# Performance work log

Measured on AMD Instinct MI355X. Metric: run time of the kernel, lower is better.

## Reference

```python
import jax, jax.numpy as jnp
from jax import lax
import numpy as np

SEQ_LEN, INPUT_DIM, HID, NCLS, BATCH = 1024, 1, 512, 10, 256


def setup_inputs() -> dict:
    key = jax.random.key(0)
    k1, k2, k3, k4 = jax.random.split(key, 4)
    def xavier(k, shape):
        fan_in, fan_out = shape[1], shape[0]
        bound = np.sqrt(6.0 / (fan_in + fan_out))
        return jax.random.uniform(k, shape, jnp.float32, -bound, bound)
    return {
        "x": jax.random.normal(k1, (BATCH, SEQ_LEN), jnp.float32),
        "h_init": jnp.zeros((HID, 1), jnp.float32),
        "W_hx": xavier(k2, (HID, INPUT_DIM)),
        "W_hh": xavier(k3, (HID, HID)),
        "b_h": jnp.zeros((HID, 1), jnp.float32),
        "W_ph": xavier(k4, (NCLS, HID)),
        "b_p": jnp.zeros((NCLS, 1), jnp.float32),
    }


def reference(x, h_init, W_hx, W_hh, b_h, W_ph, b_p):
    # x: [B, T] scalar inputs per step (input_dim == 1)
    B = x.shape[0]
    H = h_init.shape[0]
    # Broadcasting h_init [H,1] to [H,B] up-front is mathematically identical
    # to the torch code (W_hh @ h_init broadcasts against [H,B] at step 0).
    h0 = jnp.broadcast_to(h_init, (H, B))

    def step(h, x_t):
        # x_t: [B]; W_hx @ x_t[None,:] -> [H, B]
        h_new = jnp.tanh(W_hx @ x_t[None, :] + W_hh @ h + b_h)
        return h_new, None

    h_last, _ = lax.scan(step, h0, x.T)  # scan over time axis [T, B]
    p = W_ph @ h_last + b_p  # [NCLS, B]
    return p.T  # [B, NCLS]
```

## Files before the change

kernel.cpp:

```cpp
#include <hip/hip_runtime.h>


#define T_SEQ    1024
#define HID      512
#define NTHREADS 512
#define NW       8
#define NCLS     10
#define RP       8
#define PAIRS    32
#define PREG     28
#define PSTRIDE  576

typedef _Float16 half2_t __attribute__((ext_vector_type(2)));

__device__ __forceinline__ unsigned int pack2(float a, float b) {
    half2_t h = {(_Float16)a, (_Float16)b};
    return __builtin_bit_cast(unsigned int, h);
}

__device__ __forceinline__ float dot2(unsigned int w, unsigned int h, float acc) {
#if __has_builtin(__builtin_amdgcn_fdot2)
    return __builtin_amdgcn_fdot2(__builtin_bit_cast(half2_t, w),
                                  __builtin_bit_cast(half2_t, h), acc, false);
#else
    half2_t wv = __builtin_bit_cast(half2_t, w), hv = __builtin_bit_cast(half2_t, h);
    return acc + (float)wv.x * (float)hv.x + (float)wv.y * (float)hv.y;
#endif
}

__device__ __forceinline__ unsigned int bcast(unsigned int v, int lane) {
#if __has_builtin(__builtin_amdgcn_readlane)
    return __builtin_amdgcn_readlane(v, lane);
#else
    return __shfl((int)v, lane, 64);
#endif
}

__device__ __forceinline__ int pidx(int row) { return row + ((row >> 5) << 2); }

__device__ __forceinline__ float fast_tanh(float s) {
#if __has_builtin(__builtin_amdgcn_exp2f)
    float e = __builtin_amdgcn_exp2f(s * 2.885390081777927f);
#else
    float e = __expf(2.0f * s);
#endif
    return 1.0f - 2.0f / (e + 1.0f);
}

__global__ __attribute__((amdgpu_flat_work_group_size(NTHREADS, NTHREADS)))
           __attribute__((amdgpu_waves_per_eu(2, 2)))
void rnn_persist(
    const float* __restrict__ x, const float* __restrict__ h_init,
    const float* __restrict__ W_hx, const float* __restrict__ W_hh,
    const float* __restrict__ b_h, const float* __restrict__ W_ph,
    const float* __restrict__ b_p, float* __restrict__ out)
{
    __shared__ uint4    Wl4[NW * RP * 64];
    __shared__ float    part[2][NW][PSTRIDE];
    __shared__ float    x_s[T_SEQ];
    __shared__ _Float16 hs[HID];

    const int tid  = threadIdx.x;
    const int b    = blockIdx.x;
    const int w    = tid >> 6;
    const int lane = tid & 63;

    for (int i = tid; i < T_SEQ; i += NTHREADS) x_s[i] = x[(size_t)b * T_SEQ + i];

    const float whx = W_hx[tid];
    const float bh  = b_h[tid];
    const int   pi  = pidx(tid);
    hs[tid] = (_Float16)h_init[tid];

    unsigned int wreg[RP][PREG];
    #pragma unroll
    for (int r = 0; r < RP; ++r) {
        const float4* row = (const float4*)(W_hh + (size_t)(RP * lane + r) * HID + 64 * w);
        #pragma unroll
        for (int q = 0; q < 7; ++q) {
            float4 v = row[q];
            wreg[r][2 * q]     = pack2(v.x, v.y);
            wreg[r][2 * q + 1] = pack2(v.z, v.w);
        }
#if __has_builtin(__builtin_amdgcn_sched_barrier)
        __builtin_amdgcn_sched_barrier(0);
#endif
        #pragma unroll
        for (int q = 7; q < 14; ++q) {
            float4 v = row[q];
            wreg[r][2 * q]     = pack2(v.x, v.y);
            wreg[r][2 * q + 1] = pack2(v.z, v.w);
        }
        float4 v14 = row[14], v15 = row[15];
        Wl4[(w * RP + r) * 64 + lane] =
            make_uint4(pack2(v14.x, v14.y), pack2(v14.z, v14.w),
                       pack2(v15.x, v15.y), pack2(v15.z, v15.w));
#if __has_builtin(__builtin_amdgcn_sched_barrier)
        __builtin_amdgcn_sched_barrier(0);
#endif
    }

    #pragma unroll
    for (int r = 0; r < RP; ++r)
        #pragma unroll
        for (int p = 0; p < PREG; ++p)
            asm volatile("" : "+v"(wreg[r][p]));

    __syncthreads();

    const unsigned int* hs32 = (const unsigned int*)hs;
    float hval = 0.0f;

    #pragma unroll 1
    for (int t = 0; t < T_SEQ; ++t) {
        const int buf = t & 1;
        const float xw = x_s[t];

        unsigned int hpack = hs32[w * 32 + (lane & 31)];

        float acc[RP];
        #pragma unroll
        for (int r = 0; r < RP; ++r) acc[r] = 0.0f;

        #pragma unroll
        for (int p = 0; p < PREG; ++p) {
            unsigned int hp = bcast(hpack, p);
            #pragma unroll
            for (int r = 0; r < RP; ++r) acc[r] = dot2(wreg[r][p], hp, acc[r]);
        }
        {
            unsigned int hh0 = bcast(hpack, 28), hh1 = bcast(hpack, 29),
                         hh2 = bcast(hpack, 30), hh3 = bcast(hpack, 31);
            #pragma unroll
            for (int r = 0; r < RP; ++r) {
                uint4 wq = Wl4[(w * RP + r) * 64 + lane];
                acc[r] = dot2(wq.x, hh0, acc[r]);
                acc[r] = dot2(wq.y, hh1, acc[r]);
                acc[r] = dot2(wq.z, hh2, acc[r]);
                acc[r] = dot2(wq.w, hh3, acc[r]);
            }
        }

        *(float4*)&part[buf][w][pidx(RP * lane)]     = make_float4(acc[0], acc[1], acc[2], acc[3]);
        *(float4*)&part[buf][w][pidx(RP * lane + 4)] = make_float4(acc[4], acc[5], acc[6], acc[7]);

        __syncthreads();

        float s = whx * xw + bh;
        #pragma unroll
        for (int j = 0; j < NW; ++j) s += part[buf][j][pi];

        hval = fast_tanh(s);
        hs[tid] = (_Float16)hval;
    }

    __syncthreads();
    x_s[tid] = hval;
    __syncthreads();

    for (int c = w; c < NCLS; c += NW) {
        float s = 0.0f;
        #pragma unroll
        for (int j = 0; j < 8; ++j) {
            int r = lane + 64 * j;
            s += W_ph[c * HID + r] * x_s[r];
        }
        #pragma unroll
        for (int off = 32; off; off >>= 1) s += __shfl_down(s, off, 64);
        if (lane == 0) out[b * NCLS + c] = s + b_p[c];
    }
}

extern "C" void kernel_launch(void* const* d_in, const int* in_sizes, int n_in,
                              void* d_out, int out_size, void* d_ws, size_t ws_size,
                              hipStream_t stream) {
    const float* x      = (const float*)d_in[0];
    const float* h_init = (const float*)d_in[1];
    const float* W_hx   = (const float*)d_in[2];
    const float* W_hh   = (const float*)d_in[3];
    const float* b_h    = (const float*)d_in[4];
    const float* W_ph   = (const float*)d_in[5];
    const float* b_p    = (const float*)d_in[6];
    float* out = (float*)d_out;

    const int B = in_sizes[0] / T_SEQ;
    rnn_persist<<<B, NTHREADS, 0, stream>>>(x, h_init, W_hx, W_hh, b_h, W_ph, b_p, out);
}
```

Measured before the change: 1.435 ms.

## Split hidden rows between dot2 waves and MFMA waves with double-buffered state

Warps 0-3 keep the dot2 register-resident path for the first 256 hidden rows, and warps 4-7 compute the other 256 rows with 16x16x32 f16 MFMA using register-held A fragments, part of which spills to LDS. The hidden state is double-buffered in LDS and each step synchronizes with two raw s_barriers. The aim is to cut the per-step serial dot-product latency by moving half the matvec onto matrix cores and shrinking the partial-sum reduction. In exchange there are two barriers per step, MFMA waves where only one lane in 16 writes results, and a load imbalance between the two halves.

```diff
diff --git a/kernel.cpp b/kernel.cpp
--- a/kernel.cpp
+++ b/kernel.cpp
@@ -6,12 +6,25 @@
 #define NTHREADS 512
 #define NW       8
 #define NCLS     10
-#define RP       8
-#define PAIRS    32
-#define PREG     28
-#define PSTRIDE  576
+
+#define RV       256
+#define RPV      4
+#define PREG_V   56
+#define PSTRIDE  288
+
+#define NTILE    4
+#define KSTEPS   16
+#define KREG     14
 
 typedef _Float16 half2_t __attribute__((ext_vector_type(2)));
+typedef _Float16 half8_t __attribute__((ext_vector_type(8)));
+typedef float    f32x4_t __attribute__((ext_vector_type(4)));
+
+#if __has_builtin(__builtin_amdgcn_sched_barrier)
+#define SCHED_BARRIER() __builtin_amdgcn_sched_barrier(0)
+#else
+#define SCHED_BARRIER()
+#endif
 
 __device__ __forceinline__ unsigned int pack2(float a, float b) {
     half2_t h = {(_Float16)a, (_Float16)b};
@@ -47,6 +60,12 @@
     return 1.0f - 2.0f / (e + 1.0f);
 }
 
+__device__ __forceinline__ void wg_barrier() {
+    asm volatile("s_waitcnt lgkmcnt(0)" ::: "memory");
+    __builtin_amdgcn_s_barrier();
+    asm volatile("" ::: "memory");
+}
+
 __global__ __attribute__((amdgpu_flat_work_group_size(NTHREADS, NTHREADS)))
            __attribute__((amdgpu_waves_per_eu(2, 2)))
 void rnn_persist(
@@ -55,10 +74,12 @@
     const float* __restrict__ b_h, const float* __restrict__ W_ph,
     const float* __restrict__ b_p, float* __restrict__ out)
 {
-    __shared__ uint4    Wl4[NW * RP * 64];
-    __shared__ float    part[2][NW][PSTRIDE];
-    __shared__ float    x_s[T_SEQ];
-    __shared__ _Float16 hs[HID];
+    __shared__ __align__(16) float    x_s[T_SEQ];
+    __shared__ __align__(16) float    part[4][PSTRIDE];
+    __shared__ __align__(16) _Float16 hs[2][HID];
+    __shared__ uint4 WlA[4][RPV][64];
+    __shared__ uint4 WlB[4][RPV][64];
+    __shared__ uint4 Aspill[4][NTILE][2][64];
 
     const int tid  = threadIdx.x;
     const int b    = blockIdx.x;
@@ -66,96 +87,196 @@
     const int lane = tid & 63;
 
     for (int i = tid; i < T_SEQ; i += NTHREADS) x_s[i] = x[(size_t)b * T_SEQ + i];
-
-    const float whx = W_hx[tid];
-    const float bh  = b_h[tid];
-    const int   pi  = pidx(tid);
-    hs[tid] = (_Float16)h_init[tid];
-
-    unsigned int wreg[RP][PREG];
-    #pragma unroll
-    for (int r = 0; r < RP; ++r) {
-        const float4* row = (const float4*)(W_hh + (size_t)(RP * lane + r) * HID + 64 * w);
-        #pragma unroll
-        for (int q = 0; q < 7; ++q) {
-            float4 v = row[q];
-            wreg[r][2 * q]     = pack2(v.x, v.y);
-            wreg[r][2 * q + 1] = pack2(v.z, v.w);
-        }
-#if __has_builtin(__builtin_amdgcn_sched_barrier)
-        __builtin_amdgcn_sched_barrier(0);
-#endif
-        #pragma unroll
-        for (int q = 7; q < 14; ++q) {
-            float4 v = row[q];
-            wreg[r][2 * q]     = pack2(v.x, v.y);
-            wreg[r][2 * q + 1] = pack2(v.z, v.w);
-        }
-        float4 v14 = row[14], v15 = row[15];
-        Wl4[(w * RP + r) * 64 + lane] =
-            make_uint4(pack2(v14.x, v14.y), pack2(v14.z, v14.w),
-                       pack2(v15.x, v15.y), pack2(v15.z, v15.w));
-#if __has_builtin(__builtin_amdgcn_sched_barrier)
-        __builtin_amdgcn_sched_barrier(0);
-#endif
+    hs[0][tid] = (_Float16)h_init[tid];
+
+    if (w < 4) {
+        const float whx = W_hx[tid];
+        const float bh  = b_h[tid];
+        const int   pi  = pidx(tid);
+
+        unsigned int wreg[RPV][PREG_V];
+        #pragma unroll
+        for (int r = 0; r < RPV; ++r) {
+            const float* row = W_hh + (size_t)(RPV * lane + r) * HID + 128 * w;
+            #pragma unroll
+            for (int q = 0; q < 14; ++q) {
+                float4 v = *(const float4*)(row + 4 * q);
+                wreg[r][2 * q]     = pack2(v.x, v.y);
+                wreg[r][2 * q + 1] = pack2(v.z, v.w);
+            }
+            SCHED_BARRIER();
+            #pragma unroll
+            for (int q = 14; q < 28; ++q) {
+                float4 v = *(const float4*)(row + 4 * q);
+                wreg[r][2 * q]     = pack2(v.x, v.y);
+                wreg[r][2 * q + 1] = pack2(v.z, v.w);
+            }
+            float4 a0 = *(const float4*)(row + 112);
+            float4 a1 = *(const float4*)(row + 116);
+            WlA[w][r][lane] = make_uint4(pack2(a0.x, a0.y), pack2(a0.z, a0.w),
+                                         pack2(a1.x, a1.y), pack2(a1.z, a1.w));
+            float4 b0 = *(const float4*)(row + 120);
+            float4 b1 = *(const float4*)(row + 124);
+            WlB[w][r][lane] = make_uint4(pack2(b0.x, b0.y), pack2(b0.z, b0.w),
+                                         pack2(b1.x, b1.y), pack2(b1.z, b1.w));
+            SCHED_BARRIER();
+        }
+        #pragma unroll
+        for (int r = 0; r < RPV; ++r)
+            #pragma unroll
+            for (int p = 0; p < PREG_V; ++p)
+                asm volatile("" : "+v"(wreg[r][p]));
+
+        wg_barrier();
+
+        float hval = 0.0f;
+        #pragma unroll 1
+        for (int t = 0; t < T_SEQ; ++t) {
+            const int cur = t & 1;
+            const float xw = x_s[t];
+            unsigned int hpack = ((const unsigned int*)hs[cur])[64 * w + lane];
+
+            float acc[RPV] = {0.0f, 0.0f, 0.0f, 0.0f};
+            #pragma unroll
+            for (int p = 0; p < PREG_V; ++p) {
+                unsigned int hp = bcast(hpack, p);
+                #pragma unroll
+                for (int r = 0; r < RPV; ++r) acc[r] = dot2(wreg[r][p], hp, acc[r]);
+            }
+            {
+                unsigned int h0 = bcast(hpack, 56), h1 = bcast(hpack, 57),
+                             h2 = bcast(hpack, 58), h3 = bcast(hpack, 59);
+                #pragma unroll
+                for (int r = 0; r < RPV; ++r) {
+                    uint4 q = WlA[w][r][lane];
+                    acc[r] = dot2(q.x, h0, acc[r]);
+                    acc[r] = dot2(q.y, h1, acc[r]);
+                    acc[r] = dot2(q.z, h2, acc[r]);
+                    acc[r] = dot2(q.w, h3, acc[r]);
+                }
+                h0 = bcast(hpack, 60); h1 = bcast(hpack, 61);
+                h2 = bcast(hpack, 62); h3 = bcast(hpack, 63);
+                #pragma unroll
+                for (int r = 0; r < RPV; ++r) {
+                    uint4 q = WlB[w][r][lane];
+                    acc[r] = dot2(q.x, h0, acc[r]);
+                    acc[r] = dot2(q.y, h1, acc[r]);
+                    acc[r] = dot2(q.z, h2, acc[r]);
+                    acc[r] = dot2(q.w, h3, acc[r]);
+                }
+            }
+            *(float4*)&part[w][pidx(RPV * lane)] =
+                make_float4(acc[0], acc[1], acc[2], acc[3]);
+
+            wg_barrier();
+
+            float s = whx * xw + bh;
+            #pragma unroll
+            for (int j = 0; j < 4; ++j) s += part[j][pi];
+            hval = fast_tanh(s);
+            hs[cur ^ 1][tid] = (_Float16)hval;
+
+            wg_barrier();
+        }
+        x_s[tid] = hval;
+    } else {
+        const int widx  = w - 4;
+        const int g     = lane >> 4;
+        const int rloc  = lane & 15;
+        const int rbase = RV + 64 * widx;
+
+        half8_t afrag[NTILE][KREG];
+        float   whxr[NTILE][4], bhr[NTILE][4];
+        #pragma unroll
+        for (int tt = 0; tt < NTILE; ++tt) {
+            const float* rowp = W_hh + (size_t)(rbase + 16 * tt + rloc) * HID;
+            #pragma unroll
+            for (int ks = 0; ks < KREG; ++ks) {
+                float4 v0 = *(const float4*)(rowp + 32 * ks + 8 * g);
+                float4 v1 = *(const float4*)(rowp + 32 * ks + 8 * g + 4);
+                half8_t a = {(_Float16)v0.x, (_Float16)v0.y, (_Float16)v0.z, (_Float16)v0.w,
+                             (_Float16)v1.x, (_Float16)v1.y, (_Float16)v1.z, (_Float16)v1.w};
+                afrag[tt][ks] = a;
+                if (ks == 6) SCHED_BARRIER();
+            }
+            SCHED_BARRIER();
+            #pragma unroll
+            for (int ks = KREG; ks < KSTEPS; ++ks) {
+                float4 v0 = *(const float4*)(rowp + 32 * ks + 8 * g);
+                float4 v1 = *(const float4*)(rowp + 32 * ks + 8 * g + 4);
+                Aspill[widx][tt][ks - KREG][lane] =
+                    make_uint4(pack2(v0.x, v0.y), pack2(v0.z, v0.w),
+                               pack2(v1.x, v1.y), pack2(v1.z, v1.w));
+            }
+            #pragma unroll
+            for (int qq = 0; qq < 4; ++qq) {
+                const int rr = rbase + 16 * tt + 4 * g + qq;
+                whxr[tt][qq] = W_hx[rr];
+                bhr[tt][qq]  = b_h[rr];
+            }
+            SCHED_BARRIER();
+        }
+
+        f32x4_t acc[NTILE];
+        wg_barrier();
+
+        #pragma unroll 1
+        for (int t = 0; t < T_SEQ; ++t) {
+            const int cur = t & 1;
+            #pragma unroll
+            for (int tt = 0; tt < NTILE; ++tt) acc[tt] = (f32x4_t){0.f, 0.f, 0.f, 0.f};
+
+            #pragma unroll
+            for (int ks = 0; ks < KREG; ++ks) {
+                half8_t bf = *(const half8_t*)&hs[cur][32 * ks + 8 * g];
+                #pragma unroll
+                for (int tt = 0; tt < NTILE; ++tt)
+                    acc[tt] = __builtin_amdgcn_mfma_f32_16x16x32_f16(
+                                  afrag[tt][ks], bf, acc[tt], 0, 0, 0);
+            }
+            #pragma unroll
+            for (int ks = KREG; ks < KSTEPS; ++ks) {
+                half8_t bf = *(const half8_t*)&hs[cur][32 * ks + 8 * g];
+                #pragma unroll
+                for (int tt = 0; tt < NTILE; ++tt) {
+                    half8_t a = __builtin_bit_cast(half8_t,
+                                    Aspill[widx][tt][ks - KREG][lane]);
+                    acc[tt] = __builtin_amdgcn_mfma_f32_16x16x32_f16(
+                                  a, bf, acc[tt], 0, 0, 0);
+                }
+            }
+
+            const float xw = x_s[t];
+            if (rloc == 0) {
+                #pragma unroll
+                for (int tt = 0; tt < NTILE; ++tt) {
+                    float v0 = fast_tanh(acc[tt][0] + whxr[tt][0] * xw + bhr[tt][0]);
+                    float v1 = fast_tanh(acc[tt][1] + whxr[tt][1] * xw + bhr[tt][1]);
+                    float v2 = fast_tanh(acc[tt][2] + whxr[tt][2] * xw + bhr[tt][2]);
+                    float v3 = fast_tanh(acc[tt][3] + whxr[tt][3] * xw + bhr[tt][3]);
+                    *(uint2*)&hs[cur ^ 1][rbase + 16 * tt + 4 * g] =
+                        make_uint2(pack2(v0, v1), pack2(v2, v3));
+                }
+            }
+
+            wg_barrier();
+            wg_barrier();
+        }
+
+        const float xwl = x_s[T_SEQ - 1];
+        if (rloc == 0) {
+            #pragma unroll
+            for (int tt = 0; tt < NTILE; ++tt) {
+                float v0 = fast_tanh(acc[tt][0] + whxr[tt][0] * xwl + bhr[tt][0]);
+                float v1 = fast_tanh(acc[tt][1] + whxr[tt][1] * xwl + bhr[tt][1]);
+                float v2 = fast_tanh(acc[tt][2] + whxr[tt][2] * xwl + bhr[tt][2]);
+                float v3 = fast_tanh(acc[tt][3] + whxr[tt][3] * xwl + bhr[tt][3]);
+                *(float4*)&x_s[rbase + 16 * tt + 4 * g] =
+                    make_float4(v0, v1, v2, v3);
+            }
+        }
     }
 
-    #pragma unroll
-    for (int r = 0; r < RP; ++r)
-        #pragma unroll
-        for (int p = 0; p < PREG; ++p)
-            asm volatile("" : "+v"(wreg[r][p]));
-
-    __syncthreads();
-
-    const unsigned int* hs32 = (const unsigned int*)hs;
-    float hval = 0.0f;
-
-    #pragma unroll 1
-    for (int t = 0; t < T_SEQ; ++t) {
-        const int buf = t & 1;
-        const float xw = x_s[t];
-
-        unsigned int hpack = hs32[w * 32 + (lane & 31)];
-
-        float acc[RP];
-        #pragma unroll
-        for (int r = 0; r < RP; ++r) acc[r] = 0.0f;
-
-        #pragma unroll
-        for (int p = 0; p < PREG; ++p) {
-            unsigned int hp = bcast(hpack, p);
-            #pragma unroll
-            for (int r = 0; r < RP; ++r) acc[r] = dot2(wreg[r][p], hp, acc[r]);
-        }
-        {
-            unsigned int hh0 = bcast(hpack, 28), hh1 = bcast(hpack, 29),
-                         hh2 = bcast(hpack, 30), hh3 = bcast(hpack, 31);
-            #pragma unroll
-            for (int r = 0; r < RP; ++r) {
-                uint4 wq = Wl4[(w * RP + r) * 64 + lane];
-                acc[r] = dot2(wq.x, hh0, acc[r]);
-                acc[r] = dot2(wq.y, hh1, acc[r]);
-                acc[r] = dot2(wq.z, hh2, acc[r]);
-                acc[r] = dot2(wq.w, hh3, acc[r]);
-            }
-        }
-
-        *(float4*)&part[buf][w][pidx(RP * lane)]     = make_float4(acc[0], acc[1], acc[2], acc[3]);
-        *(float4*)&part[buf][w][pidx(RP * lane + 4)] = make_float4(acc[4], acc[5], acc[6], acc[7]);
-
-        __syncthreads();
-
-        float s = whx * xw + bh;
-        #pragma unroll
-        for (int j = 0; j < NW; ++j) s += part[buf][j][pi];
-
-        hval = fast_tanh(s);
-        hs[tid] = (_Float16)hval;
-    }
-
-    __syncthreads();
-    x_s[tid] = hval;
     __syncthreads();
 
     for (int c = w; c < NCLS; c += NW) {
```

New measurement: 2.474 ms. 72.4% more time.

## Batch 16 sequences per workgroup and compute recurrence with MFMA

Applied to the files above, without the earlier changes.

Replaces the per-sequence fdot2 recurrence with a 16-column batched MFMA formulation where each wave owns 64 full rows of W_hh in registers, removing the cross-wave partial-sum reduction and one barrier per step. Hidden states are double-buffered in LDS as fp16 and the input/bias term is folded into the accumulator init. Launches B/16 workgroups instead of B, so far fewer CUs are used and per-step latency depends on MFMA chain length.

```diff
diff --git a/kernel.cpp b/kernel.cpp
--- a/kernel.cpp
+++ b/kernel.cpp
@@ -6,37 +6,27 @@
 #define NTHREADS 512
 #define NW       8
 #define NCLS     10
-#define RP       8
-#define PAIRS    32
-#define PREG     28
-#define PSTRIDE  576
+#define COLS     16
+#define NTILE    4
+#define KSTEPS   16
+#define HSTR     520
+#define XSTR     1028
+#define HFSTR    516
 
 typedef _Float16 half2_t __attribute__((ext_vector_type(2)));
+typedef _Float16 half8_t __attribute__((ext_vector_type(8)));
+typedef float    f32x4_t __attribute__((ext_vector_type(4)));
+
+#if __has_builtin(__builtin_amdgcn_sched_barrier)
+#define SCHED_BARRIER() __builtin_amdgcn_sched_barrier(0)
+#else
+#define SCHED_BARRIER()
+#endif
 
 __device__ __forceinline__ unsigned int pack2(float a, float b) {
     half2_t h = {(_Float16)a, (_Float16)b};
     return __builtin_bit_cast(unsigned int, h);
 }
-
-__device__ __forceinline__ float dot2(unsigned int w, unsigned int h, float acc) {
-#if __has_builtin(__builtin_amdgcn_fdot2)
-    return __builtin_amdgcn_fdot2(__builtin_bit_cast(half2_t, w),
-                                  __builtin_bit_cast(half2_t, h), acc, false);
-#else
-    half2_t wv = __builtin_bit_cast(half2_t, w), hv = __builtin_bit_cast(half2_t, h);
-    return acc + (float)wv.x * (float)hv.x + (float)wv.y * (float)hv.y;
-#endif
-}
-
-__device__ __forceinline__ unsigned int bcast(unsigned int v, int lane) {
-#if __has_builtin(__builtin_amdgcn_readlane)
-    return __builtin_amdgcn_readlane(v, lane);
-#else
-    return __shfl((int)v, lane, 64);
-#endif
-}
-
-__device__ __forceinline__ int pidx(int row) { return row + ((row >> 5) << 2); }
 
 __device__ __forceinline__ float fast_tanh(float s) {
 #if __has_builtin(__builtin_amdgcn_exp2f)
@@ -49,125 +39,118 @@
 
 __global__ __attribute__((amdgpu_flat_work_group_size(NTHREADS, NTHREADS)))
            __attribute__((amdgpu_waves_per_eu(2, 2)))
-void rnn_persist(
+void rnn_mfma(
     const float* __restrict__ x, const float* __restrict__ h_init,
     const float* __restrict__ W_hx, const float* __restrict__ W_hh,
     const float* __restrict__ b_h, const float* __restrict__ W_ph,
     const float* __restrict__ b_p, float* __restrict__ out)
 {
-    __shared__ uint4    Wl4[NW * RP * 64];
-    __shared__ float    part[2][NW][PSTRIDE];
-    __shared__ float    x_s[T_SEQ];
-    __shared__ _Float16 hs[HID];
+    __shared__ __align__(16) _Float16 hs[2][COLS * HSTR];
+    __shared__ __align__(16) float    xs[COLS * XSTR];
+    __shared__ __align__(16) float    hfin[COLS * HFSTR];
 
     const int tid  = threadIdx.x;
-    const int b    = blockIdx.x;
     const int w    = tid >> 6;
     const int lane = tid & 63;
+    const int col  = lane & 15;
+    const int g    = lane >> 4;
+    const int col0 = blockIdx.x * COLS;
 
-    for (int i = tid; i < T_SEQ; i += NTHREADS) x_s[i] = x[(size_t)b * T_SEQ + i];
-
-    const float whx = W_hx[tid];
-    const float bh  = b_h[tid];
-    const int   pi  = pidx(tid);
-    hs[tid] = (_Float16)h_init[tid];
-
-    unsigned int wreg[RP][PREG];
-    #pragma unroll
-    for (int r = 0; r < RP; ++r) {
-        const float4* row = (const float4*)(W_hh + (size_t)(RP * lane + r) * HID + 64 * w);
-        #pragma unroll
-        for (int q = 0; q < 7; ++q) {
-            float4 v = row[q];
-            wreg[r][2 * q]     = pack2(v.x, v.y);
-            wreg[r][2 * q + 1] = pack2(v.z, v.w);
-        }
-#if __has_builtin(__builtin_amdgcn_sched_barrier)
-        __builtin_amdgcn_sched_barrier(0);
-#endif
-        #pragma unroll
-        for (int q = 7; q < 14; ++q) {
-            float4 v = row[q];
-            wreg[r][2 * q]     = pack2(v.x, v.y);
-            wreg[r][2 * q + 1] = pack2(v.z, v.w);
-        }
-        float4 v14 = row[14], v15 = row[15];
-        Wl4[(w * RP + r) * 64 + lane] =
-            make_uint4(pack2(v14.x, v14.y), pack2(v14.z, v14.w),
-                       pack2(v15.x, v15.y), pack2(v15.z, v15.w));
-#if __has_builtin(__builtin_amdgcn_sched_barrier)
-        __builtin_amdgcn_sched_barrier(0);
-#endif
+    for (int i = tid; i < COLS * T_SEQ; i += NTHREADS) {
+        const int c = i >> 10, t = i & (T_SEQ - 1);
+        xs[c * XSTR + t] = x[(size_t)(col0 + c) * T_SEQ + t];
+    }
+    for (int i = tid; i < COLS * HID; i += NTHREADS) {
+        const int c = i >> 9, r = i & (HID - 1);
+        hs[0][c * HSTR + r] = (_Float16)h_init[r];
     }
 
+    half8_t afrag[NTILE][KSTEPS];
+    float   whxr[NTILE][4], bhr[NTILE][4];
     #pragma unroll
-    for (int r = 0; r < RP; ++r)
+    for (int tt = 0; tt < NTILE; ++tt) {
+        const float* rowp = W_hh + (size_t)(64 * w + 16 * tt + col) * HID + 8 * g;
         #pragma unroll
-        for (int p = 0; p < PREG; ++p)
-            asm volatile("" : "+v"(wreg[r][p]));
+        for (int ks = 0; ks < KSTEPS; ++ks) {
+            float4 v0 = *(const float4*)(rowp + 32 * ks);
+            float4 v1 = *(const float4*)(rowp + 32 * ks + 4);
+            half8_t a = {(_Float16)v0.x, (_Float16)v0.y, (_Float16)v0.z, (_Float16)v0.w,
+                         (_Float16)v1.x, (_Float16)v1.y, (_Float16)v1.z, (_Float16)v1.w};
+            afrag[tt][ks] = a;
+            if ((ks & 3) == 3) SCHED_BARRIER();
+        }
+        #pragma unroll
+        for (int q = 0; q < 4; ++q) {
+            const int rr = 64 * w + 16 * tt + 4 * g + q;
+            whxr[tt][q] = W_hx[rr];
+            bhr[tt][q]  = b_h[rr];
+        }
+        SCHED_BARRIER();
+    }
+    #pragma unroll
+    for (int tt = 0; tt < NTILE; ++tt)
+        #pragma unroll
+        for (int ks = 0; ks < KSTEPS; ++ks)
+            asm volatile("" : "+v"(afrag[tt][ks]));
 
     __syncthreads();
 
-    const unsigned int* hs32 = (const unsigned int*)hs;
-    float hval = 0.0f;
-
     #pragma unroll 1
     for (int t = 0; t < T_SEQ; ++t) {
-        const int buf = t & 1;
-        const float xw = x_s[t];
+        const int cur = t & 1;
+        const _Float16* hb = &hs[cur][col * HSTR + 8 * g];
+        const float xw = xs[col * XSTR + t];
 
-        unsigned int hpack = hs32[w * 32 + (lane & 31)];
-
-        float acc[RP];
+        f32x4_t acc[NTILE];
         #pragma unroll
-        for (int r = 0; r < RP; ++r) acc[r] = 0.0f;
+        for (int tt = 0; tt < NTILE; ++tt) {
+            f32x4_t a0;
+            #pragma unroll
+            for (int q = 0; q < 4; ++q) a0[q] = whxr[tt][q] * xw + bhr[tt][q];
+            acc[tt] = a0;
+        }
 
         #pragma unroll
-        for (int p = 0; p < PREG; ++p) {
-            unsigned int hp = bcast(hpack, p);
+        for (int ks = 0; ks < KSTEPS; ++ks) {
+            half8_t bf = *(const half8_t*)(hb + 32 * ks);
             #pragma unroll
-            for (int r = 0; r < RP; ++r) acc[r] = dot2(wreg[r][p], hp, acc[r]);
-        }
-        {
-            unsigned int hh0 = bcast(hpack, 28), hh1 = bcast(hpack, 29),
-                         hh2 = bcast(hpack, 30), hh3 = bcast(hpack, 31);
-            #pragma unroll
-            for (int r = 0; r < RP; ++r) {
-                uint4 wq = Wl4[(w * RP + r) * 64 + lane];
-                acc[r] = dot2(wq.x, hh0, acc[r]);
-                acc[r] = dot2(wq.y, hh1, acc[r]);
-                acc[r] = dot2(wq.z, hh2, acc[r]);
-                acc[r] = dot2(wq.w, hh3, acc[r]);
-            }
+            for (int tt = 0; tt < NTILE; ++tt)
+                acc[tt] = __builtin_amdgcn_mfma_f32_16x16x32_f16(
+                              afrag[tt][ks], bf, acc[tt], 0, 0, 0);
         }
 
-        *(float4*)&part[buf][w][pidx(RP * lane)]     = make_float4(acc[0], acc[1], acc[2], acc[3]);
-        *(float4*)&part[buf][w][pidx(RP * lane + 4)] = make_float4(acc[4], acc[5], acc[6], acc[7]);
+        _Float16* hn = &hs[cur ^ 1][col * HSTR];
+        #pragma unroll
+        for (int tt = 0; tt < NTILE; ++tt) {
+            const float v0 = fast_tanh(acc[tt][0]);
+            const float v1 = fast_tanh(acc[tt][1]);
+            const float v2 = fast_tanh(acc[tt][2]);
+            const float v3 = fast_tanh(acc[tt][3]);
+            *(uint2*)&hn[64 * w + 16 * tt + 4 * g] =
+                make_uint2(pack2(v0, v1), pack2(v2, v3));
+            if (t == T_SEQ - 1)
+                *(float4*)&hfin[col * HFSTR + 64 * w + 16 * tt + 4 * g] =
+                    make_float4(v0, v1, v2, v3);
+        }
 
         __syncthreads();
-
-        float s = whx * xw + bh;
-        #pragma unroll
-        for (int j = 0; j < NW; ++j) s += part[buf][j][pi];
-
-        hval = fast_tanh(s);
-        hs[tid] = (_Float16)hval;
     }
 
-    __syncthreads();
-    x_s[tid] = hval;
-    __syncthreads();
-
-    for (int c = w; c < NCLS; c += NW) {
-        float s = 0.0f;
-        #pragma unroll
-        for (int j = 0; j < 8; ++j) {
-            int r = lane + 64 * j;
-            s += W_ph[c * HID + r] * x_s[r];
+    {
+        const int sub = lane >> 5, l32 = lane & 31;
+        const int cl  = 2 * w + sub;
+        #pragma unroll 1
+        for (int c = 0; c < NCLS; ++c) {
+            float s = 0.0f;
+            #pragma unroll
+            for (int j = 0; j < 16; ++j) {
+                const int r = l32 + 32 * j;
+                s += W_ph[c * HID + r] * hfin[cl * HFSTR + r];
+            }
+            #pragma unroll
+            for (int off = 16; off; off >>= 1) s += __shfl_down(s, off, 64);
+            if (l32 == 0) out[(size_t)(col0 + cl) * NCLS + c] = s + b_p[c];
         }
-        #pragma unroll
-        for (int off = 32; off; off >>= 1) s += __shfl_down(s, off, 64);
-        if (lane == 0) out[b * NCLS + c] = s + b_p[c];
     }
 }
 
@@ -183,6 +166,7 @@
     const float* b_p    = (const float*)d_in[6];
     float* out = (float*)d_out;
 
-    const int B = in_sizes[0] / T_SEQ;
-    rnn_persist<<<B, NTHREADS, 0, stream>>>(x, h_init, W_hx, W_hh, b_h, W_ph, b_p, out);
+    const int B   = in_sizes[0] / T_SEQ;
+    const int nwg = B / COLS;
+    rnn_mfma<<<nwg, NTHREADS, 0, stream>>>(x, h_init, W_hx, W_hh, b_h, W_ph, b_p, out);
 }
```

Measured after the change: 5.079 ms. +254.0%, slower.
